# Performance work log

Hardware: AMD Instinct MI355X
Metric: run time of the kernel (lower is better)

The kernel has to match this reference:

```python
import jax, jax.numpy as jnp
import numpy as np

VOCAB, EMB, CLASSES = 100000, 256, 100
B, S, L = 64, 128, 64


def setup_inputs() -> dict:
    key = jax.random.key(0)
    k1, k2, k3, k4, k5 = jax.random.split(key, 5)
    return {
        "tok_lists_batch": jax.random.randint(k1, (B, S, L), 0, VOCAB, dtype=jnp.int64)
        if jax.config.jax_enable_x64 else jax.random.randint(k1, (B, S, L), 0, VOCAB, dtype=jnp.int32),
        "emb_weight": jax.random.normal(k2, (VOCAB, EMB), dtype=jnp.float32),
        "class_embs": jax.random.normal(k3, (CLASSES, EMB), dtype=jnp.float32),
        "multi_weight": jax.random.normal(k4, (CLASSES, EMB), dtype=jnp.float32),
        "multi_bias": jax.random.normal(k5, (CLASSES, 1), dtype=jnp.float32),
    }


def reference(tok_lists_batch, emb_weight, class_embs, multi_weight, multi_bias):
    # EmbeddingBag(mode='mean'): gather token embeddings then mean over sent_len.
    # sents: (B, S, E)
    sents = jnp.mean(emb_weight[tok_lists_batch], axis=2)
    # attention scores: (B, C, S) = class_embs @ sents^T, softmax over sentences
    scores = jnp.einsum("ce,bse->bcs", class_embs, sents)
    atts = jax.nn.softmax(scores, axis=-1)
    # mixes: (B, C, E)
    mixes = jnp.einsum("bcs,bse->bce", atts, sents)
    # per-class linear: logits[b,c] = mixes[b,c,:] . multi_weight[c,:] + bias[c]
    logits = jnp.einsum("bce,ce->bc", mixes, multi_weight) + multi_bias[:, 0][None, :]
    return logits
```

## Files before the change

kernel.cpp:

```cpp
#include <hip/hip_runtime.h>

#define EMB   256
#define NCLS  100
#define NB    64
#define NS    128
#define NL    64

__global__ __launch_bounds__(256) void k_gather_mean(
    const int* __restrict__ tok, const float* __restrict__ emb,
    float* __restrict__ sents)
{
    const int w    = threadIdx.x >> 6;
    const int lane = threadIdx.x & 63;
    const int sid  = blockIdx.x * 4 + w;

    const int mytok = tok[(size_t)sid * NL + lane];

    float4 acc = make_float4(0.f, 0.f, 0.f, 0.f);
    for (int i = 0; i < NL; i += 8) {
        float4 v[8];
        #pragma unroll
        for (int j = 0; j < 8; ++j) {
            const int tk = __builtin_amdgcn_readlane(mytok, i + j);
            v[j] = reinterpret_cast<const float4*>(emb + (size_t)tk * EMB)[lane];
        }
        #pragma unroll
        for (int j = 0; j < 8; ++j) {
            acc.x += v[j].x; acc.y += v[j].y; acc.z += v[j].z; acc.w += v[j].w;
        }
    }
    const float s = 1.0f / NL;
    float4 r; r.x = acc.x * s; r.y = acc.y * s; r.z = acc.z * s; r.w = acc.w * s;
    reinterpret_cast<float4*>(sents + (size_t)sid * EMB)[lane] = r;
}

__device__ __forceinline__ float dot4(float4 a, float4 b) {
    return a.x * b.x + a.y * b.y + a.z * b.z + a.w * b.w;
}

#define CB    4
#define EC    32
#define SROW  36

__global__ __launch_bounds__(256) void k_attn_logits4(
    const float* __restrict__ sents, const float* __restrict__ ce,
    const float* __restrict__ mw,    const float* __restrict__ bias,
    float* __restrict__ out)
{
    const int b    = blockIdx.x;
    const int t    = threadIdx.x;
    const int lane = t & 63;
    const int c    = __builtin_amdgcn_readfirstlane(blockIdx.y * CB + (t >> 6));

    __shared__ float stile[NS][SROW];

    float sc0 = 0.f, sc1 = 0.f, tv0 = 0.f, tv1 = 0.f;

    const float* sbase = sents + (size_t)b * NS * EMB;
    const float* wrow  = ce + (size_t)c * EMB;
    const float* mrow  = mw + (size_t)c * EMB;

    for (int ec = 0; ec < EMB / EC; ++ec) {
        __syncthreads();
        {
            int i = t;
            #pragma unroll
            for (int r = 0; r < 4; ++r, i += 256) {
                const int s = i >> 3, e4 = i & 7;
                *reinterpret_cast<float4*>(&stile[s][e4 * 4]) =
                    reinterpret_cast<const float4*>(
                        sbase + (size_t)s * EMB + ec * EC)[e4];
            }
        }
        __syncthreads();

        #pragma unroll
        for (int k4 = 0; k4 < EC / 4; ++k4) {
            const float4 s0 = *reinterpret_cast<const float4*>(&stile[lane][k4 * 4]);
            const float4 s1 = *reinterpret_cast<const float4*>(&stile[lane + 64][k4 * 4]);
            const float4 w  = *reinterpret_cast<const float4*>(wrow + ec * EC + k4 * 4);
            const float4 m4 = *reinterpret_cast<const float4*>(mrow + ec * EC + k4 * 4);
            sc0 += dot4(s0, w);  sc1 += dot4(s1, w);
            tv0 += dot4(s0, m4); tv1 += dot4(s1, m4);
        }
    }

    float m = fmaxf(sc0, sc1);
    #pragma unroll
    for (int d = 1; d < 64; d <<= 1) m = fmaxf(m, __shfl_xor(m, d));
    const float p0 = __expf(sc0 - m), p1 = __expf(sc1 - m);
    float sp = p0 + p1;
    float st = p0 * tv0 + p1 * tv1;
    #pragma unroll
    for (int d = 1; d < 64; d <<= 1) {
        sp += __shfl_xor(sp, d);
        st += __shfl_xor(st, d);
    }
    if (lane == 0)
        out[(size_t)b * NCLS + c] = st / sp + bias[c];
}

extern "C" void kernel_launch(void* const* d_in, const int* in_sizes, int n_in,
                              void* d_out, int out_size, void* d_ws, size_t ws_size,
                              hipStream_t stream)
{
    const int*   tok  = (const int*)  d_in[0];
    const float* emb  = (const float*)d_in[1];
    const float* ce   = (const float*)d_in[2];
    const float* mw   = (const float*)d_in[3];
    const float* bias = (const float*)d_in[4];
    float* out   = (float*)d_out;
    float* sents = (float*)d_ws;

    k_gather_mean<<<NB * NS / 4, 256, 0, stream>>>(tok, emb, sents);
    k_attn_logits4<<<dim3(NB, NCLS / CB), 256, 0, stream>>>(sents, ce, mw, bias, out);
}
```

Before: 226.5 us.

## Split embedding chunk across waves, each wave computing all block classes

The attention kernel's work split changes. Before, each wave handled one class over the full 32-wide embedding chunk. Now each wave handles an 8-element slice of the chunk for all four classes, so every shared-memory tile element is read by only one wave and reused across four classes. Partial scores are then summed across waves through shared memory before the softmax. This cuts LDS read traffic and spreads weight loads over the waves, at the cost of more registers and an extra reduction step with two more barriers.

```diff
diff --git a/kernel.cpp b/kernel.cpp
--- a/kernel.cpp
+++ b/kernel.cpp
@@ -42,23 +42,25 @@
 #define EC    32
 #define SROW  36
 
-__global__ __launch_bounds__(256) void k_attn_logits4(
+__global__ __launch_bounds__(256) void k_attn_logits5(
     const float* __restrict__ sents, const float* __restrict__ ce,
     const float* __restrict__ mw,    const float* __restrict__ bias,
     float* __restrict__ out)
 {
     const int b    = blockIdx.x;
+    const int c0   = blockIdx.y * CB;
     const int t    = threadIdx.x;
+    const int wv   = __builtin_amdgcn_readfirstlane(t >> 6);
     const int lane = t & 63;
-    const int c    = __builtin_amdgcn_readfirstlane(blockIdx.y * CB + (t >> 6));
+    const int w8   = wv * 8;
 
     __shared__ float stile[NS][SROW];
 
-    float sc0 = 0.f, sc1 = 0.f, tv0 = 0.f, tv1 = 0.f;
+    float sc0[CB], sc1[CB], tv0[CB], tv1[CB];
+    #pragma unroll
+    for (int c = 0; c < CB; ++c) { sc0[c] = sc1[c] = tv0[c] = tv1[c] = 0.f; }
 
     const float* sbase = sents + (size_t)b * NS * EMB;
-    const float* wrow  = ce + (size_t)c * EMB;
-    const float* mrow  = mw + (size_t)c * EMB;
 
     for (int ec = 0; ec < EMB / EC; ++ec) {
         __syncthreads();
@@ -75,29 +77,54 @@
         __syncthreads();
 
         #pragma unroll
-        for (int k4 = 0; k4 < EC / 4; ++k4) {
-            const float4 s0 = *reinterpret_cast<const float4*>(&stile[lane][k4 * 4]);
-            const float4 s1 = *reinterpret_cast<const float4*>(&stile[lane + 64][k4 * 4]);
-            const float4 w  = *reinterpret_cast<const float4*>(wrow + ec * EC + k4 * 4);
-            const float4 m4 = *reinterpret_cast<const float4*>(mrow + ec * EC + k4 * 4);
-            sc0 += dot4(s0, w);  sc1 += dot4(s1, w);
-            tv0 += dot4(s0, m4); tv1 += dot4(s1, m4);
+        for (int k4 = 0; k4 < 2; ++k4) {
+            const float4 s0 = *reinterpret_cast<const float4*>(&stile[lane][w8 + k4 * 4]);
+            const float4 s1 = *reinterpret_cast<const float4*>(&stile[lane + 64][w8 + k4 * 4]);
+            #pragma unroll
+            for (int c = 0; c < CB; ++c) {
+                const size_t wo = (size_t)(c0 + c) * EMB + ec * EC + w8 + k4 * 4;
+                const float4 w4 = *reinterpret_cast<const float4*>(ce + wo);
+                const float4 m4 = *reinterpret_cast<const float4*>(mw + wo);
+                sc0[c] += dot4(s0, w4); sc1[c] += dot4(s1, w4);
+                tv0[c] += dot4(s0, m4); tv1[c] += dot4(s1, m4);
+            }
         }
     }
 
-    float m = fmaxf(sc0, sc1);
+    __syncthreads();
+    float* red = &stile[0][0];
+    #pragma unroll
+    for (int c = 0; c < CB; ++c) {
+        red[((wv * CB + c) * 2 + 0) * NS + lane]      = sc0[c];
+        red[((wv * CB + c) * 2 + 0) * NS + lane + 64] = sc1[c];
+        red[((wv * CB + c) * 2 + 1) * NS + lane]      = tv0[c];
+        red[((wv * CB + c) * 2 + 1) * NS + lane + 64] = tv1[c];
+    }
+    __syncthreads();
+
+    const int c = wv;
+    float a0 = 0.f, a1 = 0.f, q0 = 0.f, q1 = 0.f;
+    #pragma unroll
+    for (int w2 = 0; w2 < 4; ++w2) {
+        a0 += red[((w2 * CB + c) * 2 + 0) * NS + lane];
+        a1 += red[((w2 * CB + c) * 2 + 0) * NS + lane + 64];
+        q0 += red[((w2 * CB + c) * 2 + 1) * NS + lane];
+        q1 += red[((w2 * CB + c) * 2 + 1) * NS + lane + 64];
+    }
+
+    float m = fmaxf(a0, a1);
     #pragma unroll
     for (int d = 1; d < 64; d <<= 1) m = fmaxf(m, __shfl_xor(m, d));
-    const float p0 = __expf(sc0 - m), p1 = __expf(sc1 - m);
+    const float p0 = __expf(a0 - m), p1 = __expf(a1 - m);
     float sp = p0 + p1;
-    float st = p0 * tv0 + p1 * tv1;
+    float st = p0 * q0 + p1 * q1;
     #pragma unroll
     for (int d = 1; d < 64; d <<= 1) {
         sp += __shfl_xor(sp, d);
         st += __shfl_xor(st, d);
     }
     if (lane == 0)
-        out[(size_t)b * NCLS + c] = st / sp + bias[c];
+        out[(size_t)b * NCLS + c0 + c] = st / sp + bias[c0 + c];
 }
 
 extern "C" void kernel_launch(void* const* d_in, const int* in_sizes, int n_in,
@@ -113,5 +140,5 @@
     float* sents = (float*)d_ws;
 
     k_gather_mean<<<NB * NS / 4, 256, 0, stream>>>(tok, emb, sents);
-    k_attn_logits4<<<dim3(NB, NCLS / CB), 256, 0, stream>>>(sents, ce, mw, bias, out);
+    k_attn_logits5<<<dim3(NB, NCLS / CB), 256, 0, stream>>>(sents, ce, mw, bias, out);
 }
```

Measured after the change: 233.2 us. 1.03x slower.
